# Optimization experiments

Hardware: AMD Instinct MI355X
Metric: run time of the kernel (lower is better)

Reference implementation:

```python
import jax, jax.numpy as jnp
import numpy as np

B, IN, UNITS, E = 32768, 1024, 1024, 8

def setup_inputs() -> dict:
    key = jax.random.key(0)
    k1, k2, k3, k4 = jax.random.split(key, 4)
    x = jax.random.normal(k1, (B, IN), dtype=jnp.float32)
    # gate percentages: soft mixing weights over experts (sum to 1 like a softmax gate)
    gate_perc = jax.nn.softmax(jax.random.normal(k2, (B, E), dtype=jnp.float32), axis=-1)
    alpha = jax.random.normal(k3, (E, IN, UNITS), dtype=jnp.float32) * 0.05  # 'random_normal' init
    beta = jax.random.normal(k4, (E, UNITS), dtype=jnp.float32) * 0.05
    return {"x": x, "gate_perc": gate_perc, "alpha": alpha, "beta": beta}

def reference(x, gate_perc, alpha, beta):
    # Original math: w[b] = sum_e gate[b,e] * alpha[e]; bias[b] = sum_e gate[b,e] * beta[e];
    #                out = x[b] @ w[b] + bias[b]
    # Algebraically identical, avoiding the (B, IN, UNITS) per-sample weight tensor:
    # out[b,u] = sum_e gate[b,e] * (x[b] @ alpha[e])[u] + (gate @ beta)[b,u]
    out = jnp.einsum('bi,eiu,be->bu', x, alpha, gate_perc, optimize=True)
    out = out + gate_perc @ beta
    return out
```

## Files before the change

kernel.cpp:

```cpp
#include <hip/hip_runtime.h>

#define BSZ   32768
#define INF   1024
#define UNITS 1024
#define NE    8

using bf16x8 = __attribute__((ext_vector_type(8))) __bf16;
using bf16x4 = __attribute__((ext_vector_type(4))) __bf16;
using f32x4  = __attribute__((ext_vector_type(4))) float;

#define GLD_LDS16(gp, lp)                                                        \
  __builtin_amdgcn_global_load_lds((__attribute__((address_space(1))) void*)(gp),\
                                   (__attribute__((address_space(3))) void*)(lp),\
                                   16, 0, 0)

__global__ __launch_bounds__(256) void transpose_cvt(const float* __restrict__ a,
                                                     __bf16* __restrict__ at) {
  __shared__ float tile[32][33];
  const int e  = blockIdx.z;
  const int u0 = blockIdx.x * 32;
  const int i0 = blockIdx.y * 32;
  const float* src = a  + (size_t)e * (INF * UNITS);
  __bf16*      dst = at + (size_t)e * (INF * UNITS);
  const int tx = threadIdx.x & 31, ty = threadIdx.x >> 5;
#pragma unroll
  for (int r = 0; r < 32; r += 8)
    tile[ty + r][tx] = src[(size_t)(i0 + ty + r) * UNITS + (u0 + tx)];
  __syncthreads();
#pragma unroll
  for (int r = 0; r < 32; r += 8)
    dst[(size_t)(u0 + ty + r) * INF + (i0 + tx)] = (__bf16)tile[tx][ty + r];
}

__global__ __launch_bounds__(256) void cvt_x(const float* __restrict__ x,
                                             __bf16* __restrict__ xb) {
  const size_t i = ((size_t)blockIdx.x * 256 + threadIdx.x) * 8;
  f32x4 a = *(const f32x4*)(x + i);
  f32x4 b = *(const f32x4*)(x + i + 4);
  bf16x8 h;
  h[0] = (__bf16)a.x; h[1] = (__bf16)a.y; h[2] = (__bf16)a.z; h[3] = (__bf16)a.w;
  h[4] = (__bf16)b.x; h[5] = (__bf16)b.y; h[6] = (__bf16)b.z; h[7] = (__bf16)b.w;
  *(bf16x8*)(xb + i) = h;
}

__global__ __launch_bounds__(256, 3) void gemm_kernel(
    const __bf16* __restrict__ xb, const float* __restrict__ gate,
    const __bf16* __restrict__ aT, const float* __restrict__ beta,
    float* __restrict__ out) {
  __shared__ __align__(16) __bf16 lA[128 * 32];
  __shared__ __align__(16) __bf16 lB[128 * 32];
  __shared__ float lG[128 * NE];

  const int t    = threadIdx.x;
  const int wave = t >> 6;
  const int lane = t & 63;
  const int bm   = blockIdx.y * 128;
  const int bn   = blockIdx.x * 128;

  *(f32x4*)&lG[t * 4] = *(const f32x4*)&gate[(size_t)bm * NE + t * 4];

  const int rowS  = wave * 32 + (lane >> 2);
  const int koff  = (lane & 3) * 8;
  const __bf16* xsrc0 = xb + (size_t)(bm + rowS) * INF + koff;
  const __bf16* xsrc1 = xsrc0 + (size_t)16 * INF;
  const __bf16* bsrc0 = aT + (size_t)(bn + rowS) * INF + koff;
  const __bf16* bsrc1 = bsrc0 + (size_t)16 * INF;
  __bf16* lAdst0 = &lA[(wave * 32) * 32];
  __bf16* lAdst1 = &lA[(wave * 32 + 16) * 32];
  __bf16* lBdst0 = &lB[(wave * 32) * 32];
  __bf16* lBdst1 = &lB[(wave * 32 + 16) * 32];

  const int wm0 = (wave >> 1) * 64;
  const int wn0 = (wave & 1) * 64;
  const int fm  = lane & 15;
  const int fq  = (lane >> 4) * 4;
  const int fk  = (lane >> 4) * 8;

  f32x4 acc[4][4] = {};
  float gcur[4][4];

  __syncthreads();

  for (int kb = 0; kb < 256; ++kb) {
    const int e   = kb >> 5;
    const int kin = (kb & 31) * 32;

    if ((kb & 31) == 0) {
#pragma unroll
      for (int i = 0; i < 4; ++i)
#pragma unroll
        for (int r = 0; r < 4; ++r) {
          const int row = wm0 + i * 16 + fq + r;
          const float gn = lG[row * NE + e];
          if (kb) {
            const float ratio = gcur[i][r] / gn;
#pragma unroll
            for (int j = 0; j < 4; ++j) acc[i][j][r] *= ratio;
          }
          gcur[i][r] = gn;
        }
    }

    GLD_LDS16(xsrc0 + kin, lAdst0);
    GLD_LDS16(xsrc1 + kin, lAdst1);
    const size_t eoff = (size_t)e << 20;
    GLD_LDS16(bsrc0 + eoff + kin, lBdst0);
    GLD_LDS16(bsrc1 + eoff + kin, lBdst1);
    __syncthreads();

    bf16x8 af[4], bfr[4];
#pragma unroll
    for (int i = 0; i < 4; ++i)
      af[i] = *(const bf16x8*)&lA[(wm0 + i * 16 + fm) * 32 + fk];
#pragma unroll
    for (int j = 0; j < 4; ++j)
      bfr[j] = *(const bf16x8*)&lB[(wn0 + j * 16 + fm) * 32 + fk];
#pragma unroll
    for (int i = 0; i < 4; ++i)
#pragma unroll
      for (int j = 0; j < 4; ++j)
        acc[i][j] =
            __builtin_amdgcn_mfma_f32_16x16x32_bf16(af[i], bfr[j], acc[i][j], 0, 0, 0);
    __syncthreads();
  }

  float bcol[4][NE];
#pragma unroll
  for (int j = 0; j < 4; ++j) {
    const int u = bn + wn0 + j * 16 + fm;
#pragma unroll
    for (int e2 = 0; e2 < NE; ++e2) bcol[j][e2] = beta[e2 * UNITS + u];
  }
#pragma unroll
  for (int i = 0; i < 4; ++i) {
#pragma unroll
    for (int r = 0; r < 4; ++r) {
      const int row = wm0 + i * 16 + fq + r;
      const int b   = bm + row;
      float g8[NE];
#pragma unroll
      for (int e2 = 0; e2 < NE; ++e2) g8[e2] = lG[row * NE + e2];
#pragma unroll
      for (int j = 0; j < 4; ++j) {
        float bias = 0.f;
#pragma unroll
        for (int e2 = 0; e2 < NE; ++e2) bias += g8[e2] * bcol[j][e2];
        const int u = bn + wn0 + j * 16 + fm;
        out[(size_t)b * UNITS + u] = gcur[i][r] * acc[i][j][r] + bias;
      }
    }
  }
}

extern "C" void kernel_launch(void* const* d_in, const int* in_sizes, int n_in,
                              void* d_out, int out_size, void* d_ws, size_t ws_size,
                              hipStream_t stream) {
  const float* x     = (const float*)d_in[0];
  const float* gate  = (const float*)d_in[1];
  const float* alpha = (const float*)d_in[2];
  const float* beta  = (const float*)d_in[3];
  float* out         = (float*)d_out;
  __bf16* aT = (__bf16*)d_ws;
  __bf16* xbp = (__bf16*)((char*)d_ws + (size_t)16 * 1024 * 1024);

  transpose_cvt<<<dim3(UNITS / 32, INF / 32, NE), 256, 0, stream>>>(alpha, aT);
  cvt_x<<<dim3(BSZ * INF / (256 * 8)), 256, 0, stream>>>(x, xbp);
  gemm_kernel<<<dim3(UNITS / 128, BSZ / 128), 256, 0, stream>>>(xbp, gate, aT, beta, out);
}
```

Before: 918.6 us.

## Rewrite MoE GEMM with 256x256 tiles, quad-buffered swizzled LDS pipeline

Replaces the 128x128 single-buffered GEMM with a 512-thread 256x256 tile kernel that uses a four-slot LDS ring over 64-wide K stages. Global-to-LDS copies for upcoming stages are interleaved with MFMA blocks, guarded by explicit vmcnt waits and barriers. LDS rows are XOR-swizzled to reduce bank conflicts, and block indices are remapped for L2 locality. This aims to raise arithmetic intensity and hide load latency, at the cost of 136KB of LDS, which allows only one block per CU, and more complex hand-managed synchronisation.

```diff
diff --git a/kernel.cpp b/kernel.cpp
--- a/kernel.cpp
+++ b/kernel.cpp
@@ -6,7 +6,6 @@
 #define NE    8
 
 using bf16x8 = __attribute__((ext_vector_type(8))) __bf16;
-using bf16x4 = __attribute__((ext_vector_type(4))) __bf16;
 using f32x4  = __attribute__((ext_vector_type(4))) float;
 
 #define GLD_LDS16(gp, lp)                                                        \
@@ -43,110 +42,158 @@
   *(bf16x8*)(xb + i) = h;
 }
 
-__global__ __launch_bounds__(256, 3) void gemm_kernel(
+__global__ __launch_bounds__(512, 2) void gemm_kernel(
     const __bf16* __restrict__ xb, const float* __restrict__ gate,
     const __bf16* __restrict__ aT, const float* __restrict__ beta,
     float* __restrict__ out) {
-  __shared__ __align__(16) __bf16 lA[128 * 32];
-  __shared__ __align__(16) __bf16 lB[128 * 32];
-  __shared__ float lG[128 * NE];
+  __shared__ __align__(16) __bf16 lA[4][128 * 64];
+  __shared__ __align__(16) __bf16 lB[4][128 * 64];
+  __shared__ float lG[256 * NE];
 
   const int t    = threadIdx.x;
   const int wave = t >> 6;
   const int lane = t & 63;
-  const int bm   = blockIdx.y * 128;
-  const int bn   = blockIdx.x * 128;
+  const int wm   = wave >> 2;
+  const int wn   = wave & 3;
+  const int hB   = wn >> 1;
+  const int fm   = lane & 15;
+  const int kq   = lane >> 4;
+  const int fq   = kq * 4;
+  const int sw   = fm & 7;
+  const int bR   = (wn & 1) * 64 + fm;
+
+  const int li = (blockIdx.x & 7) * 64 + (blockIdx.x >> 3);
+  const int bn = (li >> 7) * 256;
+  const int bm = (li & 127) * 256;
 
   *(f32x4*)&lG[t * 4] = *(const f32x4*)&gate[(size_t)bm * NE + t * 4];
 
-  const int rowS  = wave * 32 + (lane >> 2);
-  const int koff  = (lane & 3) * 8;
-  const __bf16* xsrc0 = xb + (size_t)(bm + rowS) * INF + koff;
-  const __bf16* xsrc1 = xsrc0 + (size_t)16 * INF;
-  const __bf16* bsrc0 = aT + (size_t)(bn + rowS) * INF + koff;
-  const __bf16* bsrc1 = bsrc0 + (size_t)16 * INF;
-  __bf16* lAdst0 = &lA[(wave * 32) * 32];
-  __bf16* lAdst1 = &lA[(wave * 32 + 16) * 32];
-  __bf16* lBdst0 = &lB[(wave * 32) * 32];
-  __bf16* lBdst1 = &lB[(wave * 32 + 16) * 32];
-
-  const int wm0 = (wave >> 1) * 64;
-  const int wn0 = (wave & 1) * 64;
-  const int fm  = lane & 15;
-  const int fq  = (lane >> 4) * 4;
-  const int fk  = (lane >> 4) * 8;
-
-  f32x4 acc[4][4] = {};
-  float gcur[4][4];
-
-  __syncthreads();
-
-  for (int kb = 0; kb < 256; ++kb) {
-    const int e   = kb >> 5;
-    const int kin = (kb & 31) * 32;
-
-    if ((kb & 31) == 0) {
-#pragma unroll
-      for (int i = 0; i < 4; ++i)
-#pragma unroll
-        for (int r = 0; r < 4; ++r) {
-          const int row = wm0 + i * 16 + fq + r;
-          const float gn = lG[row * NE + e];
-          if (kb) {
-            const float ratio = gcur[i][r] / gn;
-#pragma unroll
-            for (int j = 0; j < 4; ++j) acc[i][j][r] *= ratio;
-          }
-          gcur[i][r] = gn;
-        }
-    }
-
-    GLD_LDS16(xsrc0 + kin, lAdst0);
-    GLD_LDS16(xsrc1 + kin, lAdst1);
-    const size_t eoff = (size_t)e << 20;
-    GLD_LDS16(bsrc0 + eoff + kin, lBdst0);
-    GLD_LDS16(bsrc1 + eoff + kin, lBdst1);
-    __syncthreads();
-
-    bf16x8 af[4], bfr[4];
-#pragma unroll
-    for (int i = 0; i < 4; ++i)
-      af[i] = *(const bf16x8*)&lA[(wm0 + i * 16 + fm) * 32 + fk];
-#pragma unroll
-    for (int j = 0; j < 4; ++j)
-      bfr[j] = *(const bf16x8*)&lB[(wn0 + j * 16 + fm) * 32 + fk];
-#pragma unroll
-    for (int i = 0; i < 4; ++i)
-#pragma unroll
-      for (int j = 0; j < 4; ++j)
-        acc[i][j] =
-            __builtin_amdgcn_mfma_f32_16x16x32_bf16(af[i], bfr[j], acc[i][j], 0, 0, 0);
-    __syncthreads();
+  const int stRow   = wave * 16 + (lane >> 3);
+  const int stChunk = ((lane & 7) ^ (lane >> 3)) << 3;
+  const __bf16* pA  = xb + (size_t)(bm + stRow) * INF + stChunk;
+  const __bf16* pB  = aT + (size_t)(bn + stRow) * INF + stChunk;
+
+#define STAGE_A(SLOT, KT, HF)                                                   \
+  do {                                                                          \
+    const __bf16* s_ = pA + (size_t)(HF) * (128 * INF) + (((KT) & 15) << 6);    \
+    GLD_LDS16(s_, &lA[SLOT][(wave * 16) * 64]);                                 \
+    GLD_LDS16(s_ + 8 * INF, &lA[SLOT][(wave * 16 + 8) * 64]);                   \
+  } while (0)
+
+#define STAGE_B(SLOT, KT, HF)                                                   \
+  do {                                                                          \
+    const __bf16* s_ = pB + ((size_t)((KT) >> 4) << 20) +                       \
+                       (size_t)(HF) * (128 * INF) + (((KT) & 15) << 6);         \
+    GLD_LDS16(s_, &lB[SLOT][(wave * 16) * 64]);                                 \
+    GLD_LDS16(s_ + 8 * INF, &lB[SLOT][(wave * 16 + 8) * 64]);                   \
+  } while (0)
+
+#define LDAF(SLOT, ROW, C) \
+  (*(const bf16x8*)&lA[SLOT][((ROW) << 6) + ((((C) ^ sw)) << 3)])
+#define LDBF(SLOT, ROW, C) \
+  (*(const bf16x8*)&lB[SLOT][((ROW) << 6) + ((((C) ^ sw)) << 3)])
+
+#define LOAD_B(SLOT)                                    \
+  _Pragma("unroll") for (int n = 0; n < 4; ++n) {       \
+    bq[n][0] = LDBF(SLOT, bR + n * 16, kq);             \
+    bq[n][1] = LDBF(SLOT, bR + n * 16, 4 + kq);         \
+  }
+
+#define LOAD_A(SLOT, Q)                                        \
+  _Pragma("unroll") for (int mm = 0; mm < 2; ++mm) {           \
+    aq[mm][0] = LDAF(SLOT, (Q) * 32 + mm * 16 + fm, kq);       \
+    aq[mm][1] = LDAF(SLOT, (Q) * 32 + mm * 16 + fm, 4 + kq);   \
+  }
+
+#define VMW(N) asm volatile("s_waitcnt vmcnt(" #N ")" ::: "memory")
+
+#define MFMA_BLK(Q)                                                            \
+  do {                                                                         \
+    __builtin_amdgcn_s_barrier();                                              \
+    asm volatile("s_waitcnt lgkmcnt(0)" ::: "memory");                         \
+    __builtin_amdgcn_s_setprio(1);                                             \
+    _Pragma("unroll") for (int mm = 0; mm < 2; ++mm)                           \
+    _Pragma("unroll") for (int n = 0; n < 4; ++n) {                            \
+      acc[(Q) * 2 + mm][n] = __builtin_amdgcn_mfma_f32_16x16x32_bf16(          \
+          aq[mm][0], bq[n][0], acc[(Q) * 2 + mm][n], 0, 0, 0);                 \
+      acc[(Q) * 2 + mm][n] = __builtin_amdgcn_mfma_f32_16x16x32_bf16(          \
+          aq[mm][1], bq[n][1], acc[(Q) * 2 + mm][n], 0, 0, 0);                 \
+    }                                                                          \
+    __builtin_amdgcn_s_setprio(0);                                             \
+    __builtin_amdgcn_s_barrier();                                              \
+    asm volatile("" ::: "memory");                                             \
+  } while (0)
+
+#define RESCALE(E)                                                 \
+  do {                                                             \
+    _Pragma("unroll") for (int m = 0; m < 8; ++m)                  \
+    _Pragma("unroll") for (int r = 0; r < 4; ++r) {                \
+      const int rowL  = wm * 128 + m * 16 + fq + r;                \
+      const float go  = lG[rowL * NE + (E)-1];                     \
+      const float gn  = lG[rowL * NE + (E)];                       \
+      const float ra  = go / gn;                                   \
+      _Pragma("unroll") for (int n = 0; n < 4; ++n)                \
+        acc[m][n][r] *= ra;                                        \
+    }                                                              \
+  } while (0)
+
+  bf16x8 aq[2][2], bq[4][2];
+  f32x4  acc[8][4] = {};
+
+  STAGE_B(0, 0, 0); STAGE_B(1, 0, 1);
+  STAGE_A(0, 0, 0); STAGE_A(1, 0, 1);
+  STAGE_B(2, 1, 0); STAGE_B(3, 1, 1);
+  asm volatile("s_waitcnt vmcnt(4) lgkmcnt(0)" ::: "memory");
+  __builtin_amdgcn_s_barrier();
+  asm volatile("" ::: "memory");
+
+#pragma unroll 1
+  for (int i = 0; i < 63; ++i) {
+    if (i && !(i & 7)) RESCALE(i >> 3);
+    const int kt1 = 2 * i + 1, ktn = 2 * i + 2, ktn1 = 2 * i + 3;
+    LOAD_B(hB);     LOAD_A(wm, 0);     STAGE_A(2, kt1, 0);           MFMA_BLK(0);
+                    LOAD_A(wm, 1);     STAGE_A(3, kt1, 1);           MFMA_BLK(1);
+                    LOAD_A(wm, 2);     STAGE_B(0, ktn, 0);           MFMA_BLK(2);
+                    LOAD_A(wm, 3);     STAGE_B(1, ktn, 1);  VMW(4);  MFMA_BLK(3);
+    LOAD_B(2 + hB); LOAD_A(2 + wm, 0); STAGE_A(0, ktn, 0);           MFMA_BLK(0);
+                    LOAD_A(2 + wm, 1); STAGE_A(1, ktn, 1);           MFMA_BLK(1);
+                    LOAD_A(2 + wm, 2); STAGE_B(2, ktn1, 0);          MFMA_BLK(2);
+                    LOAD_A(2 + wm, 3); STAGE_B(3, ktn1, 1); VMW(4);  MFMA_BLK(3);
+  }
+  {
+    LOAD_B(hB);     LOAD_A(wm, 0);     STAGE_A(2, 127, 0);           MFMA_BLK(0);
+                    LOAD_A(wm, 1);     STAGE_A(3, 127, 1);           MFMA_BLK(1);
+                    LOAD_A(wm, 2);                                   MFMA_BLK(2);
+                    LOAD_A(wm, 3);                          VMW(0);  MFMA_BLK(3);
+    LOAD_B(2 + hB); LOAD_A(2 + wm, 0);                               MFMA_BLK(0);
+                    LOAD_A(2 + wm, 1);                               MFMA_BLK(1);
+                    LOAD_A(2 + wm, 2);                               MFMA_BLK(2);
+                    LOAD_A(2 + wm, 3);                               MFMA_BLK(3);
   }
 
   float bcol[4][NE];
 #pragma unroll
-  for (int j = 0; j < 4; ++j) {
-    const int u = bn + wn0 + j * 16 + fm;
-#pragma unroll
-    for (int e2 = 0; e2 < NE; ++e2) bcol[j][e2] = beta[e2 * UNITS + u];
-  }
-#pragma unroll
-  for (int i = 0; i < 4; ++i) {
+  for (int n = 0; n < 4; ++n) {
+    const int u = bn + wn * 64 + n * 16 + fm;
+#pragma unroll
+    for (int e2 = 0; e2 < NE; ++e2) bcol[n][e2] = beta[e2 * UNITS + u];
+  }
+#pragma unroll
+  for (int m = 0; m < 8; ++m) {
 #pragma unroll
     for (int r = 0; r < 4; ++r) {
-      const int row = wm0 + i * 16 + fq + r;
-      const int b   = bm + row;
+      const int rowL = wm * 128 + m * 16 + fq + r;
+      const int b    = bm + rowL;
       float g8[NE];
 #pragma unroll
-      for (int e2 = 0; e2 < NE; ++e2) g8[e2] = lG[row * NE + e2];
-#pragma unroll
-      for (int j = 0; j < 4; ++j) {
+      for (int e2 = 0; e2 < NE; ++e2) g8[e2] = lG[rowL * NE + e2];
+#pragma unroll
+      for (int n = 0; n < 4; ++n) {
         float bias = 0.f;
 #pragma unroll
-        for (int e2 = 0; e2 < NE; ++e2) bias += g8[e2] * bcol[j][e2];
-        const int u = bn + wn0 + j * 16 + fm;
-        out[(size_t)b * UNITS + u] = gcur[i][r] * acc[i][j][r] + bias;
+        for (int e2 = 0; e2 < NE; ++e2) bias += g8[e2] * bcol[n][e2];
+        const int u = bn + wn * 64 + n * 16 + fm;
+        out[(size_t)b * UNITS + u] = g8[7] * acc[m][n][r] + bias;
       }
     }
   }
@@ -160,10 +207,10 @@
   const float* alpha = (const float*)d_in[2];
   const float* beta  = (const float*)d_in[3];
   float* out         = (float*)d_out;
-  __bf16* aT = (__bf16*)d_ws;
+  __bf16* aT  = (__bf16*)d_ws;
   __bf16* xbp = (__bf16*)((char*)d_ws + (size_t)16 * 1024 * 1024);
 
   transpose_cvt<<<dim3(UNITS / 32, INF / 32, NE), 256, 0, stream>>>(alpha, aT);
   cvt_x<<<dim3(BSZ * INF / (256 * 8)), 256, 0, stream>>>(x, xbp);
-  gemm_kernel<<<dim3(UNITS / 128, BSZ / 128), 256, 0, stream>>>(xbp, gate, aT, beta, out);
-}
+  gemm_kernel<<<dim3(512), 512, 0, stream>>>(xbp, gate, aT, beta, out);
+}
```

Measured after the change: 752.3 us. 18.1% less time.
